# Optimization experiments

Hardware: AMD Instinct MI355X
Metric: run time of the kernel (lower is better)

## Reference

```python
import jax, jax.numpy as jnp
import numpy as np

B, N, D = 8, 4096, 512
NUM_CODES = 8192

def setup_inputs() -> dict:
    key = jax.random.key(0)
    kx, kc = jax.random.split(key)
    x = jax.random.normal(kx, (B, N, D), dtype=jnp.float32)
    codebook = jax.random.normal(kc, (NUM_CODES, D), dtype=jnp.float32)
    return {"x": x, "codebook": codebook}

def reference(x, codebook):
    # x: (B, N, D); codebook: (K, D)
    b = x.shape[0]
    flat = x.reshape(-1, x.shape[-1])  # (B*N, D)
    distances = (
        jnp.sum(flat * flat, axis=1, keepdims=True)
        + jnp.sum(codebook * codebook, axis=1)
        - 2.0 * flat @ codebook.T
    )
    codes = jnp.argmin(distances, axis=1).reshape(b, -1)  # (B, N) int
    return codes
```

## Files before the change

### kernel.cpp

```cpp
#include <hip/hip_runtime.h>
#include <hip/hip_bf16.h>
#include <hip/hip_fp16.h>


#define M_ROWS 32768
#define DDIM   512
#define KCODES 8192
#define NCAND  8

typedef unsigned long long u64;
typedef unsigned int u32;
typedef __attribute__((ext_vector_type(4))) float f32x4;
typedef __attribute__((ext_vector_type(8))) int v8i;

#define GL2LDS(gp, lp) __builtin_amdgcn_global_load_lds(                  \
    (const __attribute__((address_space(1))) void*)(gp),                  \
    (__attribute__((address_space(3))) void*)(lp), 16, 0, 0)

__device__ __forceinline__ u32 umin32(u32 a, u32 b) { return a < b ? a : b; }
__device__ __forceinline__ u32 umax32(u32 a, u32 b) { return a > b ? a : b; }
__device__ __forceinline__ u64 umin64(u64 a, u64 b) { return a < b ? a : b; }

__device__ __forceinline__ u32 fsort(float s) {
  u32 fb = __float_as_uint(s);
  return fb ^ (u32)(((int)fb >> 31) | 0x80000000);
}

__device__ __forceinline__ uint2 pk8_fp8(float4 v0, float4 v1) {
  int lo = 0, hi = 0;
  lo = __builtin_amdgcn_cvt_pk_fp8_f32(v0.x, v0.y, lo, false);
  lo = __builtin_amdgcn_cvt_pk_fp8_f32(v0.z, v0.w, lo, true);
  hi = __builtin_amdgcn_cvt_pk_fp8_f32(v1.x, v1.y, hi, false);
  hi = __builtin_amdgcn_cvt_pk_fp8_f32(v1.z, v1.w, hi, true);
  return (uint2){(u32)lo, (u32)hi};
}

__global__ __launch_bounds__(256) void conv_codebook_kernel(
    const float* __restrict__ cb, unsigned char* __restrict__ ch8,
    float* __restrict__ cnh) {
  int wave = (blockIdx.x * 256 + threadIdx.x) >> 6;
  int lane = threadIdx.x & 63;
  if (wave >= KCODES) return;
  const float* src = cb + (size_t)wave * DDIM + lane * 8;
  float4 v0 = *(const float4*)(src);
  float4 v1 = *(const float4*)(src + 4);
  *(uint2*)(ch8 + (size_t)wave * DDIM + lane * 8) = pk8_fp8(v0, v1);
  float ss = v0.x*v0.x + v0.y*v0.y + v0.z*v0.z + v0.w*v0.w
           + v1.x*v1.x + v1.y*v1.y + v1.z*v1.z + v1.w*v1.w;
#pragma unroll
  for (int off = 32; off; off >>= 1) ss += __shfl_xor(ss, off);
  if (lane == 0) cnh[wave] = 0.5f * ss;
}

__global__ __launch_bounds__(256) void conv_x_kernel(
    const float* __restrict__ x, unsigned char* __restrict__ xh8) {
  size_t i = ((size_t)blockIdx.x * 256 + threadIdx.x) * 8;
  float4 v0 = *(const float4*)(x + i);
  float4 v1 = *(const float4*)(x + i + 4);
  *(uint2*)(xh8 + i) = pk8_fp8(v0, v1);
}

__device__ __forceinline__ v8i ld_frag(const char* L, int row, int g) {
  const int base = row * 128;
  const int sl = ((g * 2) ^ (row & 7)) * 16;
  int4 lo = *(const int4*)&L[base + sl];
  int4 hi = *(const int4*)&L[base + (sl ^ 16)];
  v8i r;
  r[0] = lo.x; r[1] = lo.y; r[2] = lo.z; r[3] = lo.w;
  r[4] = hi.x; r[5] = hi.y; r[6] = hi.z; r[7] = hi.w;
  return r;
}

__global__ __launch_bounds__(256) void coarse_kernel(
    const unsigned char* __restrict__ xh8, const unsigned char* __restrict__ ch8,
    const float* __restrict__ cnh, uint4* __restrict__ part) {
  __shared__ __align__(16) char smem[34816];
  char* aL = smem;
  char* bL = smem + 16384;
  uint4* tab = (uint4*)smem;

  const int tid  = threadIdx.x;
  const int lane = tid & 63;
  const int wid  = tid >> 6;
  const int wm   = wid >> 1, wn = wid & 1;
  const int g    = lane >> 4, l16 = lane & 15;

  const int mblk = blockIdx.x & 255;
  const int nblk = blockIdx.x >> 8;
  const int row0 = mblk * 128;
  const int col0 = nblk * 128;

  const int a_ = lane >> 3, b_ = lane & 7;
  const size_t gsrc = (size_t)a_ * DDIM + ((b_ ^ a_) << 4);

  f32x4 acc[4][4];
#pragma unroll
  for (int tm = 0; tm < 4; ++tm)
#pragma unroll
    for (int tn = 0; tn < 4; ++tn) acc[tm][tn] = (f32x4){0.f, 0.f, 0.f, 0.f};

#pragma unroll
  for (int c = 0; c < 4; ++c) {
    __syncthreads();
#pragma unroll
    for (int j = 0; j < 4; ++j) {
      const int I = wid * 4 + j;
      const size_t off = (size_t)(I * 8) * DDIM + c * 128 + gsrc;
      GL2LDS(xh8 + (size_t)row0 * DDIM + off, aL + I * 1024);
      GL2LDS(ch8 + (size_t)col0 * DDIM + off, bL + I * 1024);
    }
    __syncthreads();

    v8i af[4];
#pragma unroll
    for (int t = 0; t < 4; ++t)
      af[t] = ld_frag(aL, wm * 64 + t * 16 + l16, g);
#pragma unroll
    for (int tn = 0; tn < 4; ++tn) {
      v8i bf = ld_frag(bL, wn * 64 + tn * 16 + l16, g);
#pragma unroll
      for (int tm = 0; tm < 4; ++tm)
        acc[tm][tn] = __builtin_amdgcn_mfma_scale_f32_16x16x128_f8f6f4(
            af[tm], bf, acc[tm][tn],
            0, 0,
            0, 0x7F7F7F7F,
            0, 0x7F7F7F7F);
    }
  }

  u32 codev[4];
  float cn[4];
#pragma unroll
  for (int tn = 0; tn < 4; ++tn) {
    codev[tn] = (u32)(col0 + wn * 64 + tn * 16 + l16);
    cn[tn] = cnh[codev[tn]];
  }

  u32 k1[16], k2[16], k3[16];
#pragma unroll
  for (int tm = 0; tm < 4; ++tm)
#pragma unroll
    for (int r = 0; r < 4; ++r) {
      const int sl = tm * 4 + r;
      k1[sl] = ~0u; k2[sl] = ~0u; k3[sl] = ~0u;
#pragma unroll
      for (int tn = 0; tn < 4; ++tn) {
        float s = cn[tn] - acc[tm][tn][r];
        u32 key = (__float_as_uint(s) & 0xFFFFE000u) | codev[tn];
        u32 t1 = umax32(k1[sl], key); k1[sl] = umin32(k1[sl], key);
        u32 t2 = umax32(k2[sl], t1);  k2[sl] = umin32(k2[sl], t1);
        k3[sl] = umin32(k3[sl], t2);
      }
    }

  u32 m1 = ~0u, m2 = ~0u, m3 = ~0u;
#pragma unroll
  for (int p = 0; p < 2; ++p) {
    __syncthreads();
    if (wn == p) {
#pragma unroll
      for (int tm = 0; tm < 4; ++tm)
#pragma unroll
        for (int r = 0; r < 4; ++r) {
          const int row = wm * 64 + tm * 16 + g * 4 + r;
          const int sl = tm * 4 + r;
          tab[row * 17 + l16] = (uint4){k1[sl], k2[sl], k3[sl], 0u};
        }
    }
    __syncthreads();
    if (tid < 128) {
#pragma unroll
      for (int e = 0; e < 16; ++e) {
        uint4 v = tab[tid * 17 + e];
        u32 t1 = umax32(m1, v.x); m1 = umin32(m1, v.x);
        u32 t2 = umax32(m2, t1);  m2 = umin32(m2, t1);
        m3 = umin32(m3, t2);
        t1 = umax32(m2, v.y);     m2 = umin32(m2, v.y);
        m3 = umin32(m3, t1);
        m3 = umin32(m3, v.z);
      }
    }
  }

  if (tid < 128)
    part[(size_t)nblk * M_ROWS + row0 + tid] = (uint4){m1, m2, m3, 0u};
}

__global__ __launch_bounds__(256) void merge_kernel(
    const uint4* __restrict__ part, int* __restrict__ cand) {
  const int row = blockIdx.x * 256 + threadIdx.x;
  u32 k[NCAND];
#pragma unroll
  for (int i = 0; i < NCAND; ++i) k[i] = ~0u;
  for (int nb = 0; nb < KCODES / 128; ++nb) {
    uint4 e = part[(size_t)nb * M_ROWS + row];
    u32 t = e.x;
#pragma unroll
    for (int i = 0; i < NCAND; ++i) { u32 mx = umax32(k[i], t); k[i] = umin32(k[i], t); t = mx; }
    t = e.y;
#pragma unroll
    for (int i = 0; i < NCAND; ++i) { u32 mx = umax32(k[i], t); k[i] = umin32(k[i], t); t = mx; }
    t = e.z;
#pragma unroll
    for (int i = 0; i < NCAND; ++i) { u32 mx = umax32(k[i], t); k[i] = umin32(k[i], t); t = mx; }
  }
#pragma unroll
  for (int i = 0; i < NCAND; ++i)
    cand[row * NCAND + i] = (int)(k[i] & 0x1FFFu);
}

__global__ __launch_bounds__(256) void rescore_kernel(
    const float* __restrict__ x, const float* __restrict__ cb,
    const float* __restrict__ cnh, const int* __restrict__ cand,
    int* __restrict__ out) {
  int wave = (blockIdx.x * 256 + threadIdx.x) >> 6;
  int lane = threadIdx.x & 63;
  if (wave >= M_ROWS) return;
  int idx[NCAND];
#pragma unroll
  for (int j = 0; j < NCAND; ++j) idx[j] = cand[wave * NCAND + j];

  const float* xr = x + (size_t)wave * DDIM + lane * 8;
  float4 x0 = *(const float4*)(xr);
  float4 x1 = *(const float4*)(xr + 4);

  float d[NCAND];
#pragma unroll
  for (int j = 0; j < NCAND; ++j) {
    const float* c = cb + (size_t)idx[j] * DDIM + lane * 8;
    float4 a0 = *(const float4*)(c);
    float4 a1 = *(const float4*)(c + 4);
    d[j] = x0.x*a0.x + x0.y*a0.y + x0.z*a0.z + x0.w*a0.w
         + x1.x*a1.x + x1.y*a1.y + x1.z*a1.z + x1.w*a1.w;
  }
#pragma unroll
  for (int off = 32; off; off >>= 1)
#pragma unroll
    for (int j = 0; j < NCAND; ++j) d[j] += __shfl_xor(d[j], off);

  if (lane == 0) {
    u64 best = ~0ull;
#pragma unroll
    for (int j = 0; j < NCAND; ++j) {
      float s = cnh[idx[j]] - d[j];
      u64 key = ((u64)fsort(s) << 32) | (u32)idx[j];
      best = umin64(best, key);
    }
    out[wave] = (int)(u32)best;
  }
}

extern "C" void kernel_launch(void* const* d_in, const int* in_sizes, int n_in,
                              void* d_out, int out_size, void* d_ws, size_t ws_size,
                              hipStream_t stream) {
  const float* x  = (const float*)d_in[0];
  const float* cb = (const float*)d_in[1];
  int* out = (int*)d_out;

  char* ws = (char*)d_ws;
  unsigned char* ch8  = (unsigned char*)(ws);
  unsigned char* xh8  = (unsigned char*)(ws + (size_t)4 * 1024 * 1024);
  float*         cnh  = (float*)(ws + (size_t)20 * 1024 * 1024);
  int*           cand = (int*)(ws + (size_t)20 * 1024 * 1024 + 32 * 1024);
  uint4*         part = (uint4*)(ws + (size_t)22 * 1024 * 1024);

  conv_codebook_kernel<<<KCODES / 4, 256, 0, stream>>>(cb, ch8, cnh);
  conv_x_kernel<<<(M_ROWS * DDIM) / (256 * 8), 256, 0, stream>>>(x, xh8);
  coarse_kernel<<<(M_ROWS / 128) * (KCODES / 128), 256, 0, stream>>>(xh8, ch8, cnh, part);
  merge_kernel<<<M_ROWS / 256, 256, 0, stream>>>(part, cand);
  rescore_kernel<<<M_ROWS / 4, 256, 0, stream>>>(x, cb, cnh, cand, out);
}
```

Before: 383.5 us.

## Widen coarse FP8 GEMM tile to 256 codes and fuse conversion kernels

The coarse distance kernel now covers 256 codebook columns per block instead of 128. Each wave holds a 4x8 grid of MFMA accumulators, and the shared codebook tile grows to 32 KB. This halves the number of partial top-3 records that merge_kernel must scan and doubles reuse of each loaded x tile. The codebook and x FP8 conversion kernels are also merged into one launch. The larger tile raises register and LDS pressure, which may lower occupancy, and the top-3 candidates now come from a wider column set per partial.

```diff
diff --git a/kernel.cpp b/kernel.cpp
--- a/kernel.cpp
+++ b/kernel.cpp
@@ -35,29 +35,29 @@
   return (uint2){(u32)lo, (u32)hi};
 }
 
-__global__ __launch_bounds__(256) void conv_codebook_kernel(
-    const float* __restrict__ cb, unsigned char* __restrict__ ch8,
+__global__ __launch_bounds__(256) void conv_kernel(
+    const float* __restrict__ cb, const float* __restrict__ x,
+    unsigned char* __restrict__ ch8, unsigned char* __restrict__ xh8,
     float* __restrict__ cnh) {
-  int wave = (blockIdx.x * 256 + threadIdx.x) >> 6;
+  int w = (blockIdx.x * 256 + threadIdx.x) >> 6;
   int lane = threadIdx.x & 63;
-  if (wave >= KCODES) return;
-  const float* src = cb + (size_t)wave * DDIM + lane * 8;
-  float4 v0 = *(const float4*)(src);
-  float4 v1 = *(const float4*)(src + 4);
-  *(uint2*)(ch8 + (size_t)wave * DDIM + lane * 8) = pk8_fp8(v0, v1);
-  float ss = v0.x*v0.x + v0.y*v0.y + v0.z*v0.z + v0.w*v0.w
-           + v1.x*v1.x + v1.y*v1.y + v1.z*v1.z + v1.w*v1.w;
-#pragma unroll
-  for (int off = 32; off; off >>= 1) ss += __shfl_xor(ss, off);
-  if (lane == 0) cnh[wave] = 0.5f * ss;
-}
-
-__global__ __launch_bounds__(256) void conv_x_kernel(
-    const float* __restrict__ x, unsigned char* __restrict__ xh8) {
-  size_t i = ((size_t)blockIdx.x * 256 + threadIdx.x) * 8;
-  float4 v0 = *(const float4*)(x + i);
-  float4 v1 = *(const float4*)(x + i + 4);
-  *(uint2*)(xh8 + i) = pk8_fp8(v0, v1);
+  if (w < KCODES) {
+    const float* src = cb + (size_t)w * DDIM + lane * 8;
+    float4 v0 = *(const float4*)(src);
+    float4 v1 = *(const float4*)(src + 4);
+    *(uint2*)(ch8 + (size_t)w * DDIM + lane * 8) = pk8_fp8(v0, v1);
+    float ss = v0.x*v0.x + v0.y*v0.y + v0.z*v0.z + v0.w*v0.w
+             + v1.x*v1.x + v1.y*v1.y + v1.z*v1.z + v1.w*v1.w;
+#pragma unroll
+    for (int off = 32; off; off >>= 1) ss += __shfl_xor(ss, off);
+    if (lane == 0) cnh[w] = 0.5f * ss;
+  } else {
+    int r = w - KCODES;
+    const float* src = x + (size_t)r * DDIM + lane * 8;
+    float4 v0 = *(const float4*)(src);
+    float4 v1 = *(const float4*)(src + 4);
+    *(uint2*)(xh8 + (size_t)r * DDIM + lane * 8) = pk8_fp8(v0, v1);
+  }
 }
 
 __device__ __forceinline__ v8i ld_frag(const char* L, int row, int g) {
@@ -74,7 +74,7 @@
 __global__ __launch_bounds__(256) void coarse_kernel(
     const unsigned char* __restrict__ xh8, const unsigned char* __restrict__ ch8,
     const float* __restrict__ cnh, uint4* __restrict__ part) {
-  __shared__ __align__(16) char smem[34816];
+  __shared__ __align__(16) char smem[49152];
   char* aL = smem;
   char* bL = smem + 16384;
   uint4* tab = (uint4*)smem;
@@ -88,16 +88,16 @@
   const int mblk = blockIdx.x & 255;
   const int nblk = blockIdx.x >> 8;
   const int row0 = mblk * 128;
-  const int col0 = nblk * 128;
+  const int col0 = nblk * 256;
 
   const int a_ = lane >> 3, b_ = lane & 7;
   const size_t gsrc = (size_t)a_ * DDIM + ((b_ ^ a_) << 4);
 
-  f32x4 acc[4][4];
+  f32x4 acc[4][8];
 #pragma unroll
   for (int tm = 0; tm < 4; ++tm)
 #pragma unroll
-    for (int tn = 0; tn < 4; ++tn) acc[tm][tn] = (f32x4){0.f, 0.f, 0.f, 0.f};
+    for (int tn = 0; tn < 8; ++tn) acc[tm][tn] = (f32x4){0.f, 0.f, 0.f, 0.f};
 
 #pragma unroll
   for (int c = 0; c < 4; ++c) {
@@ -105,9 +105,14 @@
 #pragma unroll
     for (int j = 0; j < 4; ++j) {
       const int I = wid * 4 + j;
-      const size_t off = (size_t)(I * 8) * DDIM + c * 128 + gsrc;
-      GL2LDS(xh8 + (size_t)row0 * DDIM + off, aL + I * 1024);
-      GL2LDS(ch8 + (size_t)col0 * DDIM + off, bL + I * 1024);
+      GL2LDS(xh8 + (size_t)row0 * DDIM + (size_t)(I * 8) * DDIM + c * 128 + gsrc,
+             aL + I * 1024);
+    }
+#pragma unroll
+    for (int j = 0; j < 8; ++j) {
+      const int I = wid * 8 + j;
+      GL2LDS(ch8 + (size_t)col0 * DDIM + (size_t)(I * 8) * DDIM + c * 128 + gsrc,
+             bL + I * 1024);
     }
     __syncthreads();
 
@@ -116,8 +121,8 @@
     for (int t = 0; t < 4; ++t)
       af[t] = ld_frag(aL, wm * 64 + t * 16 + l16, g);
 #pragma unroll
-    for (int tn = 0; tn < 4; ++tn) {
-      v8i bf = ld_frag(bL, wn * 64 + tn * 16 + l16, g);
+    for (int tn = 0; tn < 8; ++tn) {
+      v8i bf = ld_frag(bL, wn * 128 + tn * 16 + l16, g);
 #pragma unroll
       for (int tm = 0; tm < 4; ++tm)
         acc[tm][tn] = __builtin_amdgcn_mfma_scale_f32_16x16x128_f8f6f4(
@@ -128,11 +133,11 @@
     }
   }
 
-  u32 codev[4];
-  float cn[4];
-#pragma unroll
-  for (int tn = 0; tn < 4; ++tn) {
-    codev[tn] = (u32)(col0 + wn * 64 + tn * 16 + l16);
+  u32 codev[8];
+  float cn[8];
+#pragma unroll
+  for (int tn = 0; tn < 8; ++tn) {
+    codev[tn] = (u32)(col0 + wn * 128 + tn * 16 + l16);
     cn[tn] = cnh[codev[tn]];
   }
 
@@ -144,7 +149,7 @@
       const int sl = tm * 4 + r;
       k1[sl] = ~0u; k2[sl] = ~0u; k3[sl] = ~0u;
 #pragma unroll
-      for (int tn = 0; tn < 4; ++tn) {
+      for (int tn = 0; tn < 8; ++tn) {
         float s = cn[tn] - acc[tm][tn][r];
         u32 key = (__float_as_uint(s) & 0xFFFFE000u) | codev[tn];
         u32 t1 = umax32(k1[sl], key); k1[sl] = umin32(k1[sl], key);
@@ -192,7 +197,7 @@
   u32 k[NCAND];
 #pragma unroll
   for (int i = 0; i < NCAND; ++i) k[i] = ~0u;
-  for (int nb = 0; nb < KCODES / 128; ++nb) {
+  for (int nb = 0; nb < KCODES / 256; ++nb) {
     uint4 e = part[(size_t)nb * M_ROWS + row];
     u32 t = e.x;
 #pragma unroll
@@ -264,9 +269,8 @@
   int*           cand = (int*)(ws + (size_t)20 * 1024 * 1024 + 32 * 1024);
   uint4*         part = (uint4*)(ws + (size_t)22 * 1024 * 1024);
 
-  conv_codebook_kernel<<<KCODES / 4, 256, 0, stream>>>(cb, ch8, cnh);
-  conv_x_kernel<<<(M_ROWS * DDIM) / (256 * 8), 256, 0, stream>>>(x, xh8);
-  coarse_kernel<<<(M_ROWS / 128) * (KCODES / 128), 256, 0, stream>>>(xh8, ch8, cnh, part);
+  conv_kernel<<<(KCODES + M_ROWS) / 4, 256, 0, stream>>>(cb, x, ch8, xh8, cnh);
+  coarse_kernel<<<(M_ROWS / 128) * (KCODES / 256), 256, 0, stream>>>(xh8, ch8, cnh, part);
   merge_kernel<<<M_ROWS / 256, 256, 0, stream>>>(part, cand);
   rescore_kernel<<<M_ROWS / 4, 256, 0, stream>>>(x, cb, cnh, cand, out);
 }
```

Result: slower. 434.1 us (+13.2%).
